# Optimization experiments

Hardware: AMD Instinct MI355X
Metric: run time of the kernel (lower is better)

## Reference

```python
import jax, jax.numpy as jnp
import numpy as np

B, N, H, R = 128, 512, 256, 3
VIRTUAL_DECAY = 0.7


def _build_tree():
    # Deterministic random recursive tree: parent[i] ~ U[0, i)
    rng = np.random.default_rng(0)
    parent = np.zeros(N, np.int64)
    for i in range(1, N):
        parent[i] = rng.integers(0, i)
    depth = np.zeros(N, np.int64)
    for i in range(1, N):
        depth[i] = depth[parent[i]] + 1
    rel_edge = rng.integers(0, R, N)          # relation type of edge (parent -> i)
    virtual = rng.random(N) < 0.1
    children = [[] for _ in range(N)]
    for i in range(1, N):
        children[parent[i]].append(i)
    # Group internal nodes by depth (deepest first == valid post-order batching),
    # pad ragged child lists per level.
    levels = []
    for d in range(int(depth.max()), -1, -1):
        nodes = [n for n in range(N) if depth[n] == d and len(children[n]) > 0]
        if not nodes:
            continue
        cmax = max(len(children[n]) for n in nodes)
        M = len(nodes)
        cidx = np.zeros((M, cmax), np.int64)
        cmask = np.zeros((M, cmax), np.float32)
        crel = np.zeros((M, cmax), np.int64)
        cvirt = np.zeros((M, cmax), bool)
        for m, n in enumerate(nodes):
            ch = children[n]
            k = len(ch)
            cidx[m, :k] = ch
            cmask[m, :k] = 1.0
            crel[m, :k] = rel_edge[ch]
            cvirt[m, :k] = virtual[ch]
        levels.append((jnp.array(nodes), jnp.array(cidx), jnp.array(cmask),
                       jnp.array(crel), jnp.array(cvirt)))
    return levels

LEVELS = _build_tree()


def _forward(node_features, W_enc, b_enc, rel_emb, W_i, b_i, W_o, b_o, W_u, b_u,
             W_f, b_f, w_attn, b_attn):
    h = node_features @ W_enc + b_enc            # (B, N, H) node_encoder
    c = jnp.zeros_like(h)
    for node_ids, cidx, cmask, crel, cvirt in LEVELS:
        x = h[:, node_ids]                       # (B, M, H) input_vec (== encoded feats)
        ch_h = h[:, cidx]                        # (B, M, C, H)
        ch_c = c[:, cidx]
        # virtual-node decay + padding mask
        decay = jnp.where(cvirt, VIRTUAL_DECAY, 1.0).astype(h.dtype) * cmask  # (M, C)
        ch_h = ch_h * decay[None, :, :, None]
        ch_c = ch_c * decay[None, :, :, None]
        # relation-aware attention over children
        re = rel_emb[crel]                       # (M, C, H)
        scores = jnp.einsum('bmch,h->bmc', re[None] + ch_h, w_attn) + b_attn[0]
        scores = jnp.where(cmask[None] > 0, scores, -1e9)
        attw = jax.nn.softmax(scores, axis=-1)   # (B, M, C)
        h_sum = jnp.einsum('bmc,bmch->bmh', attw, ch_h)
        # per-relation forget transform (note: original applies NO sigmoid here)
        f = jnp.zeros_like(ch_h)
        for r in range(R):
            fr = jnp.einsum('bmch,hk->bmck', ch_h, W_f[r]) + b_f[r]
            f = f + fr * (crel == r).astype(h.dtype)[None, :, :, None]
        c_sum = jnp.sum(f * ch_c, axis=2)        # (B, M, H); padded ch_c is 0
        comb = jnp.concatenate([x, h_sum], axis=-1)  # (B, M, 2H)
        i_g = jax.nn.sigmoid(comb @ W_i + b_i)
        o_g = jax.nn.sigmoid(comb @ W_o + b_o)
        u_g = jnp.tanh(comb @ W_u + b_u)
        c_new = i_g * u_g + c_sum
        h_new = o_g * jnp.tanh(c_new)
        h = h.at[:, node_ids].set(h_new)
        c = c.at[:, node_ids].set(c_new)
    return h[:, 0]                               # pooling == 'root' (root = 0)


def setup_inputs() -> dict:
    key = jax.random.key(0)
    ks = jax.random.split(key, 8)
    s = 0.05
    f32 = jnp.float32
    return {
        'node_features': jax.random.normal(ks[0], (B, N, H), f32),
        'W_enc': jax.random.normal(ks[1], (H, H), f32) * s,
        'b_enc': jnp.full((H,), 0.1, f32),
        'rel_emb': jax.random.normal(ks[2], (R, H), f32) * s,
        'W_i': jax.random.normal(ks[3], (2 * H, H), f32) * s,
        'b_i': jnp.full((H,), 0.1, f32),
        'W_o': jax.random.normal(ks[4], (2 * H, H), f32) * s,
        'b_o': jnp.full((H,), 0.1, f32),
        'W_u': jax.random.normal(ks[5], (2 * H, H), f32) * s,
        'b_u': jnp.full((H,), 0.1, f32),
        'W_f': jax.random.normal(ks[6], (R, H, H), f32) * s,
        'b_f': jnp.full((R, H), 0.1, f32),
        'w_attn': jax.random.normal(ks[7], (H,), f32) * s,
        'b_attn': jnp.full((1,), 0.1, f32),
    }


def reference(node_features, W_enc, b_enc, rel_emb, W_i, b_i, W_o, b_o, W_u, b_u,
              W_f, b_f, w_attn, b_attn):
    return _forward(node_features, W_enc, b_enc, rel_emb, W_i, b_i, W_o, b_o,
                    W_u, b_u, W_f, b_f, w_attn, b_attn)
```

## Files before the change

kernel.cpp:

```cpp
#include <hip/hip_runtime.h>
#include <stdint.h>
#include <string.h>
#include <math.h>

#define NB 128
#define NN 512
#define NH 256
#define NR 3

typedef __attribute__((ext_vector_type(8))) short bh8;
typedef __attribute__((ext_vector_type(4))) float f32x4;

struct Pcg {
  __uint128_t state, inc;
  bool has32; uint32_t buf32;
};

static const __uint128_t PCG_MULT =
    (((__uint128_t)2549297995355413924ULL) << 64) | 4865540595714422341ULL;

static inline uint64_t pcg_next64(Pcg& s) {
  s.state = s.state * PCG_MULT + s.inc;
  uint64_t hi = (uint64_t)(s.state >> 64), lo = (uint64_t)s.state;
  uint64_t x = hi ^ lo;
  unsigned rot = (unsigned)(s.state >> 122) & 63u;
  return (x >> rot) | (x << ((64u - rot) & 63u));
}
static inline uint32_t pcg_next32(Pcg& s) {
  if (s.has32) { s.has32 = false; return s.buf32; }
  uint64_t n = pcg_next64(s);
  s.has32 = true; s.buf32 = (uint32_t)(n >> 32);
  return (uint32_t)n;
}
static inline uint64_t pcg_bounded(Pcg& s, uint64_t high) {
  uint64_t rng = high - 1;
  if (rng == 0) return 0;
  uint32_t rng_excl = (uint32_t)rng + 1u;
  uint64_t m = (uint64_t)pcg_next32(s) * (uint64_t)rng_excl;
  uint32_t leftover = (uint32_t)m;
  if (leftover < rng_excl) {
    uint32_t threshold = (uint32_t)((0xFFFFFFFFu - (uint32_t)rng) % rng_excl);
    while (leftover < threshold) {
      m = (uint64_t)pcg_next32(s) * (uint64_t)rng_excl;
      leftover = (uint32_t)m;
    }
  }
  return m >> 32;
}
static inline double pcg_double(Pcg& s) {
  return (double)(pcg_next64(s) >> 11) * (1.0 / 9007199254740992.0);
}

static void pcg_seed0(Pcg& s) {
  uint32_t pool[4];
  uint32_t hc = 0x43b0d7e5u;
  auto hashmix = [&hc](uint32_t v) -> uint32_t {
    v ^= hc; hc *= 0x931e8875u; v *= hc; v ^= v >> 16; return v;
  };
  auto mix = [](uint32_t x, uint32_t y) -> uint32_t {
    uint32_t r = 0xca01f9ddu * x - 0x4973f715u * y; r ^= r >> 16; return r;
  };
  for (int i = 0; i < 4; i++) pool[i] = hashmix(0u);
  for (int src = 0; src < 4; src++)
    for (int dst = 0; dst < 4; dst++)
      if (src != dst) pool[dst] = mix(pool[dst], hashmix(pool[src]));
  uint32_t gs[8]; uint32_t hb = 0x8b51f9ddu;
  for (int i = 0; i < 8; i++) {
    uint32_t dv = pool[i & 3];
    dv ^= hb; hb *= 0x58f38dedu; dv *= hb; dv ^= dv >> 16;
    gs[i] = dv;
  }
  uint64_t w0 = (uint64_t)gs[0] | ((uint64_t)gs[1] << 32);
  uint64_t w1 = (uint64_t)gs[2] | ((uint64_t)gs[3] << 32);
  uint64_t w2 = (uint64_t)gs[4] | ((uint64_t)gs[5] << 32);
  uint64_t w3 = (uint64_t)gs[6] | ((uint64_t)gs[7] << 32);
  __uint128_t initstate = (((__uint128_t)w0) << 64) | w1;
  __uint128_t initseq   = (((__uint128_t)w2) << 64) | w3;
  s.state = 0;
  s.inc = (initseq << 1) | 1;
  s.state = s.state * PCG_MULT + s.inc;
  s.state += initstate;
  s.state = s.state * PCG_MULT + s.inc;
  s.has32 = false; s.buf32 = 0;
}

struct TreeMeta {
  int nodes[512];
  int cstart[512];
  int ccount[512];
  int echild[512];
  int erel[512];
  float edecay[512];
  int cechild[512];
  int cerel[512];
  float cedec[512];
  int cens[513];
};
struct HostTree {
  TreeMeta meta;
  int n_levels;
  int level_off[520];
  int level_M[520];
};

static void build_tree_host(HostTree& T) {
  Pcg st; pcg_seed0(st);
  int parent[NN], depth[NN], rel[NN];
  unsigned char virt[NN];
  parent[0] = 0; depth[0] = 0;
  for (int i = 1; i < NN; i++) parent[i] = (int)pcg_bounded(st, (uint64_t)i);
  for (int i = 1; i < NN; i++) depth[i] = depth[parent[i]] + 1;
  for (int i = 0; i < NN; i++) rel[i] = (int)pcg_bounded(st, (uint64_t)NR);
  for (int i = 0; i < NN; i++) virt[i] = (pcg_double(st) < 0.1) ? 1 : 0;

  int childcnt[NN]; memset(childcnt, 0, sizeof(childcnt));
  for (int i = 1; i < NN; i++) childcnt[parent[i]]++;
  int maxd = 0;
  for (int i = 0; i < NN; i++) if (depth[i] > maxd) maxd = depth[i];

  int ni = 0, ne = 0, nec = 0;
  T.n_levels = 0;
  for (int d = maxd; d >= 0; d--) {
    int mstart = ni;
    for (int n = 0; n < NN; n++) {
      if (depth[n] == d && childcnt[n] > 0) {
        T.meta.nodes[ni] = n;
        T.meta.cstart[ni] = ne;
        T.meta.ccount[ni] = childcnt[n];
        T.meta.cens[ni] = nec;
        for (int i2 = 1; i2 < NN; i2++) {
          if (parent[i2] == n) {
            T.meta.echild[ne] = i2;
            T.meta.erel[ne] = rel[i2];
            T.meta.edecay[ne] = virt[i2] ? 0.7f : 1.0f;
            ne++;
            if (childcnt[i2] > 0) {
              T.meta.cechild[nec] = i2;
              T.meta.cerel[nec] = rel[i2];
              T.meta.cedec[nec] = virt[i2] ? 0.7f : 1.0f;
              nec++;
            }
          }
        }
        ni++;
      }
    }
    if (ni > mstart) {
      T.level_off[T.n_levels] = mstart;
      T.level_M[T.n_levels] = ni - mstart;
      T.n_levels++;
    }
  }
  T.meta.cens[ni] = nec;
}

__device__ __forceinline__ uint16_t f2bf(float f) {
  uint32_t u = __float_as_uint(f);
  return (uint16_t)((u + 0x7fffu + ((u >> 16) & 1u)) >> 16);
}
__device__ __forceinline__ float bf2f(uint16_t b) {
  return __uint_as_float(((uint32_t)b) << 16);
}
__device__ __forceinline__ float sigm(float x) {
  return 1.f / (1.f + expf(-x));
}

__device__ __forceinline__ void stage_bf16(uint16_t* __restrict__ sm,
    const uint16_t* __restrict__ src, int stride, int rows) {
  const int chunks = rows << 3;
  for (int cch = threadIdx.x; cch < chunks; cch += 256) {
    const int row = cch >> 3, k = (cch & 7) << 3;
    uint4 v = *(const uint4*)(src + (size_t)row * stride + k);
    *(uint4*)(sm + (((row << 6) + k) ^ ((row & 7) << 3))) = v;
  }
}
__device__ __forceinline__ void stage_f32(uint16_t* __restrict__ sm,
    const float* __restrict__ src, int stride, int rows) {
  const int chunks = rows << 3;
  for (int cch = threadIdx.x; cch < chunks; cch += 256) {
    const int row = cch >> 3, k = (cch & 7) << 3;
    const float* p = src + (size_t)row * stride + k;
    float4 a = *(const float4*)p, b = *(const float4*)(p + 4);
    uint4 w;
    w.x = (uint32_t)f2bf(a.x) | ((uint32_t)f2bf(a.y) << 16);
    w.y = (uint32_t)f2bf(a.z) | ((uint32_t)f2bf(a.w) << 16);
    w.z = (uint32_t)f2bf(b.x) | ((uint32_t)f2bf(b.y) << 16);
    w.w = (uint32_t)f2bf(b.z) | ((uint32_t)f2bf(b.w) << 16);
    *(uint4*)(sm + (((row << 6) + k) ^ ((row & 7) << 3))) = w;
  }
}
__device__ __forceinline__ bh8 fld(const uint16_t* __restrict__ sm, int row, int k) {
  return *(const bh8*)(sm + (((row << 6) + k) ^ ((row & 7) << 3)));
}

__global__ __launch_bounds__(256) void k_prep(const float* __restrict__ We,
    const float* __restrict__ Wf, const float* __restrict__ Wi,
    const float* __restrict__ Wo, const float* __restrict__ Wu,
    uint16_t* __restrict__ WeT, uint16_t* __restrict__ WfT,
    uint16_t* __restrict__ WgT) {
  const int i = blockIdx.x * 256 + threadIdx.x;
  if (i < 65536) {
    const int n = i >> 8, k = i & 255;
    WeT[i] = f2bf(We[k * 256 + n]);
  }
  const int i2 = i - 65536;
  if (i2 >= 0 && i2 < 196608) {
    const int r = i2 >> 16, rem = i2 & 65535, n = rem >> 8, k = rem & 255;
    WfT[i2] = f2bf(Wf[r * 65536 + k * 256 + n]);
  }
  const int i3 = i - 262144;
  if (i3 >= 0 && i3 < 393216) {
    const int g = i3 >> 17, rem = i3 & 131071, n = rem >> 9, k = rem & 511;
    const float* S = (g == 0) ? Wi : (g == 1) ? Wo : Wu;
    WgT[i3] = f2bf(S[k * 256 + n]);
  }
}

__global__ __launch_bounds__(256) void k_enc(const float* __restrict__ nf,
    const uint16_t* __restrict__ WeT, const float* __restrict__ b_enc,
    uint16_t* __restrict__ h_bf) {
  __shared__ __align__(16) uint16_t smA[128 * 64];
  __shared__ __align__(16) uint16_t smB[128 * 64];
  const int bm = blockIdx.x * 128, bn = blockIdx.y * 128;
  const int tid = threadIdx.x, wid = tid >> 6, lane = tid & 63;
  const int wr = wid >> 1, wc2 = wid & 1, lr = lane & 15, lk = (lane >> 4) << 3;
  f32x4 acc[4][4] = {};
  for (int k0 = 0; k0 < 256; k0 += 64) {
    __syncthreads();
    stage_f32(smA, nf + (size_t)bm * NH + k0, NH, 128);
    stage_bf16(smB, WeT + (size_t)bn * 256 + k0, 256, 128);
    __syncthreads();
#pragma unroll
    for (int ks = 0; ks < 2; ks++) {
      bh8 af[4], bfr[4];
#pragma unroll
      for (int i = 0; i < 4; i++) af[i] = fld(smA, wr * 64 + i * 16 + lr, ks * 32 + lk);
#pragma unroll
      for (int j = 0; j < 4; j++) bfr[j] = fld(smB, wc2 * 64 + j * 16 + lr, ks * 32 + lk);
#pragma unroll
      for (int i = 0; i < 4; i++)
#pragma unroll
        for (int j = 0; j < 4; j++)
          acc[i][j] = __builtin_amdgcn_mfma_f32_16x16x32_bf16(af[i], bfr[j], acc[i][j], 0, 0, 0);
    }
  }
#pragma unroll
  for (int i = 0; i < 4; i++) {
#pragma unroll
    for (int j = 0; j < 4; j++) {
      const int col = bn + wc2 * 64 + j * 16 + (lane & 15);
      const float be = b_enc[col];
#pragma unroll
      for (int r = 0; r < 4; r++) {
        const int row = bm + wr * 64 + i * 16 + (lane >> 4) * 4 + r;
        h_bf[(size_t)row * NH + col] = f2bf(acc[i][j][r] + be);
      }
    }
  }
}

__global__ __launch_bounds__(256) void k_lvl(
    uint16_t* h_bf, float* c,
    const uint16_t* __restrict__ WfT, const uint16_t* __restrict__ WgT,
    const float* __restrict__ b_f, const float* __restrict__ b_i,
    const float* __restrict__ b_o, const float* __restrict__ b_u,
    const float* __restrict__ rel_emb, const float* __restrict__ w_attn,
    const float* __restrict__ b_attn, float* __restrict__ out,
    const TreeMeta* __restrict__ tm, int nb) {
  __shared__ float sc[64 * 65];
  __shared__ float swa[256];
  __shared__ float sRE[3];
  __shared__ int chl[64]; __shared__ int rll[64]; __shared__ float dcl[64];
  __shared__ __align__(16) uint16_t hsum[4 * 4096];

  const int bx = blockIdx.x, mloc = bx >> 1, b0 = (bx & 1) * 64;
  const int cslice = blockIdx.y * 64;
  const int gi = nb + mloc;
  const int nd = tm->nodes[gi], cs = tm->cstart[gi], cc = tm->ccount[gi];
  const int ce0 = tm->cens[gi], nic = tm->cens[gi + 1] - ce0;
  const int tid = threadIdx.x, wid = tid >> 6, lane = tid & 63;
  const int lr2 = lane & 15, hi4 = (lane >> 4), lk = hi4 << 3;
  const int colw = cslice + wid * 16 + lr2;

  if (tid < cc) {
    chl[tid] = tm->echild[cs + tid];
    rll[tid] = tm->erel[cs + tid];
    dcl[tid] = tm->edecay[cs + tid];
  }
  swa[tid] = w_attn[tid];
  if (wid < 3) {
    float p = 0.f;
#pragma unroll
    for (int i = 0; i < 4; i++) p += rel_emb[wid * NH + lane + 64 * i] * w_attn[lane + 64 * i];
#pragma unroll
    for (int off = 32; off; off >>= 1) p += __shfl_down(p, off);
    if (lane == 0) sRE[wid] = p;
  }
  __syncthreads();

  const int sb = tid >> 2, sq = tid & 3;
  const float ba = b_attn[0];
  for (int e = 0; e < cc; e++) {
    const uint16_t* hp = h_bf + ((size_t)(b0 + sb) * NN + chl[e]) * NH + sq * 64;
    float s = 0.f;
#pragma unroll
    for (int v = 0; v < 8; v++) {
      uint4 pk = *(const uint4*)(hp + v * 8);
      const uint16_t* pe = (const uint16_t*)&pk;
#pragma unroll
      for (int q = 0; q < 8; q++) s = fmaf(bf2f(pe[q]), swa[sq * 64 + v * 8 + q], s);
    }
    s += __shfl_xor(s, 1); s += __shfl_xor(s, 2);
    if (sq == 0) sc[sb * 65 + e] = sRE[rll[e]] + dcl[e] * s + ba;
  }
  __syncthreads();
  if (tid < 64) {
    float mx = -1e30f;
    for (int e = 0; e < cc; e++) mx = fmaxf(mx, sc[tid * 65 + e]);
    float ss = 0.f;
    for (int e = 0; e < cc; e++) ss += expf(sc[tid * 65 + e] - mx);
    const float inv = 1.0f / ss;
    for (int e = 0; e < cc; e++) sc[tid * 65 + e] = expf(sc[tid * 65 + e] - mx) * inv * dcl[e];
  }
  __syncthreads();

  {
    float hs[64];
#pragma unroll
    for (int v = 0; v < 64; v++) hs[v] = 0.f;
    for (int e = 0; e < cc; e++) {
      const float w = sc[sb * 65 + e];
      const uint16_t* hp = h_bf + ((size_t)(b0 + sb) * NN + chl[e]) * NH + sq * 64;
#pragma unroll
      for (int v = 0; v < 8; v++) {
        uint4 pk = *(const uint4*)(hp + v * 8);
        const uint16_t* pe = (const uint16_t*)&pk;
#pragma unroll
        for (int q = 0; q < 8; q++) hs[v * 8 + q] = fmaf(bf2f(pe[q]), w, hs[v * 8 + q]);
      }
    }
    uint16_t* sub = hsum + sq * 4096;
#pragma unroll
    for (int v = 0; v < 32; v++) {
      uint32_t pk = (uint32_t)f2bf(hs[2 * v]) | ((uint32_t)f2bf(hs[2 * v + 1]) << 16);
      const int elem = ((sb << 6) + 2 * v) ^ ((sb & 7) << 3);
      *(uint32_t*)(sub + elem) = pk;
    }
  }

  f32x4 csum[4] = {};
  for (int e = 0; e < nic; e++) {
    const int ch = tm->cechild[ce0 + e];
    const int rel = tm->cerel[ce0 + e];
    const float dec = tm->cedec[ce0 + e];
    const uint16_t* Wr = WfT + (size_t)rel * 65536 + (size_t)colw * 256;
    f32x4 facc[4] = {};
#pragma unroll
    for (int k0 = 0; k0 < 8; k0++) {
      const int kk = k0 * 32 + lk;
      bh8 af[4];
#pragma unroll
      for (int i = 0; i < 4; i++)
        af[i] = *(const bh8*)(h_bf + ((size_t)(b0 + i * 16 + lr2) * NN + ch) * NH + kk);
      const bh8 bq = *(const bh8*)(Wr + kk);
#pragma unroll
      for (int i = 0; i < 4; i++)
        facc[i] = __builtin_amdgcn_mfma_f32_16x16x32_bf16(af[i], bq, facc[i], 0, 0, 0);
    }
    const float bfv = b_f[rel * NH + colw];
#pragma unroll
    for (int i = 0; i < 4; i++) {
#pragma unroll
      for (int r = 0; r < 4; r++) {
        const int brow = b0 + i * 16 + hi4 * 4 + r;
        const float cch = c[((size_t)brow * NN + ch) * NH + colw];
        csum[i][r] += (dec * facc[i][r] + bfv) * (dec * cch);
      }
    }
  }
  __syncthreads();

  f32x4 ga[3][4] = {};
#pragma unroll
  for (int k32 = 0; k32 < 16; k32++) {
    const int kk = k32 * 32 + lk;
    bh8 af[4], bq[3];
    if (k32 < 8) {
#pragma unroll
      for (int i = 0; i < 4; i++)
        af[i] = *(const bh8*)(h_bf + ((size_t)(b0 + i * 16 + lr2) * NN + nd) * NH + kk);
    } else {
      const int kx = k32 - 8;
#pragma unroll
      for (int i = 0; i < 4; i++)
        af[i] = fld(hsum + (kx >> 1) * 4096, i * 16 + lr2, (kx & 1) * 32 + lk);
    }
#pragma unroll
    for (int g = 0; g < 3; g++)
      bq[g] = *(const bh8*)(WgT + ((size_t)g << 17) + (size_t)colw * 512 + kk);
#pragma unroll
    for (int g = 0; g < 3; g++)
#pragma unroll
      for (int i = 0; i < 4; i++)
        ga[g][i] = __builtin_amdgcn_mfma_f32_16x16x32_bf16(af[i], bq[g], ga[g][i], 0, 0, 0);
  }

  const float bi_ = b_i[colw], bo_ = b_o[colw], bu_ = b_u[colw];
#pragma unroll
  for (int i = 0; i < 4; i++) {
#pragma unroll
    for (int r = 0; r < 4; r++) {
      const int brow = b0 + i * 16 + hi4 * 4 + r;
      const size_t idx = ((size_t)brow * NN + nd) * NH + colw;
      const float ig = sigm(ga[0][i][r] + bi_);
      const float og = sigm(ga[1][i][r] + bo_);
      const float ug = tanhf(ga[2][i][r] + bu_);
      const float cn = fmaf(ig, ug, csum[i][r]);
      c[idx] = cn;
      const float hn = og * tanhf(cn);
      h_bf[idx] = f2bf(hn);
      if (nd == 0) out[(size_t)brow * NH + colw] = hn;
    }
  }
}

extern "C" void kernel_launch(void* const* d_in, const int* in_sizes, int n_in,
                              void* d_out, int out_size, void* d_ws, size_t ws_size,
                              hipStream_t stream) {
  (void)in_sizes; (void)n_in; (void)out_size; (void)ws_size;
  const float* nf      = (const float*)d_in[0];
  const float* W_enc   = (const float*)d_in[1];
  const float* b_enc   = (const float*)d_in[2];
  const float* rel_emb = (const float*)d_in[3];
  const float* W_i     = (const float*)d_in[4];
  const float* b_i     = (const float*)d_in[5];
  const float* W_o     = (const float*)d_in[6];
  const float* b_o     = (const float*)d_in[7];
  const float* W_u     = (const float*)d_in[8];
  const float* b_u     = (const float*)d_in[9];
  const float* W_f     = (const float*)d_in[10];
  const float* b_f     = (const float*)d_in[11];
  const float* w_attn  = (const float*)d_in[12];
  const float* b_attn  = (const float*)d_in[13];
  float* out = (float*)d_out;

  static HostTree T;
  build_tree_host(T);

  char* ws = (char*)d_ws;
  const size_t OFF_HBF = 32768;
  const size_t SZ_HBF  = (size_t)NB * NN * NH * 2;
  const size_t OFF_WET = OFF_HBF + SZ_HBF;
  const size_t OFF_WFT = OFF_WET + 131072;
  const size_t OFF_WGT = OFF_WFT + 393216;
  const size_t OFF_C   = OFF_WGT + 786432;

  TreeMeta* dm = (TreeMeta*)ws;
  uint16_t* h_bf = (uint16_t*)(ws + OFF_HBF);
  uint16_t* WeT = (uint16_t*)(ws + OFF_WET);
  uint16_t* WfT = (uint16_t*)(ws + OFF_WFT);
  uint16_t* WgT = (uint16_t*)(ws + OFF_WGT);
  float* c = (float*)(ws + OFF_C);

  hipMemcpyAsync(dm, &T.meta, sizeof(TreeMeta), hipMemcpyHostToDevice, stream);

  k_prep<<<2560, 256, 0, stream>>>(W_enc, W_f, W_i, W_o, W_u, WeT, WfT, WgT);
  k_enc<<<dim3((NB * NN) / 128, 2), 256, 0, stream>>>(nf, WeT, b_enc, h_bf);

  for (int l = 0; l < T.n_levels; l++) {
    const int Mfull = T.level_M[l];
    for (int c0 = 0; c0 < Mfull; c0 += 128) {
      const int Mc = (Mfull - c0) < 128 ? (Mfull - c0) : 128;
      k_lvl<<<dim3(2 * Mc, 4), 256, 0, stream>>>(h_bf, c, WfT, WgT,
          b_f, b_i, b_o, b_u, rel_emb, w_attn, b_attn, out, dm,
          T.level_off[l] + c0);
    }
  }
}
```

Before: 735.5 us.

## Fuse small tree levels into one persistent tail kernel processing nodes sequentially

Consecutive levels with fewer than TH_TAIL internal nodes are handled by a new k_tail kernel, launched with 8 blocks of 16 batch rows each. Each block loops over those nodes in dependency order, computing the attention scores, the softmax-weighted child sum, the forget-gate cell sum and the gate GEMMs inside one launch. The aim is to remove the per-level launch overhead and the underutilised tiny grids of the top levels of the tree. In exchange, the tail runs on only 8 workgroups and processes its nodes serially, with repeated weight reads from global memory.

```diff
diff --git a/kernel.cpp b/kernel.cpp
--- a/kernel.cpp
+++ b/kernel.cpp
@@ -7,6 +7,7 @@
 #define NN 512
 #define NH 256
 #define NR 3
+#define TH_TAIL 10
 
 typedef __attribute__((ext_vector_type(8))) short bh8;
 typedef __attribute__((ext_vector_type(4))) float f32x4;
@@ -424,6 +425,182 @@
   }
 }
 
+__global__ __launch_bounds__(256) void k_tail(
+    uint16_t* h_bf, float* c,
+    const uint16_t* __restrict__ WfT, const uint16_t* __restrict__ WgT,
+    const float* __restrict__ b_f, const float* __restrict__ b_i,
+    const float* __restrict__ b_o, const float* __restrict__ b_u,
+    const float* __restrict__ rel_emb, const float* __restrict__ w_attn,
+    const float* __restrict__ b_attn, float* __restrict__ out,
+    const TreeMeta* __restrict__ tm, int start, int count) {
+  __shared__ float sc[16 * 68];
+  __shared__ float swaf[256];
+  __shared__ float sRE[3];
+  __shared__ int chl[64]; __shared__ int rll[64]; __shared__ float dcl[64];
+  __shared__ __align__(16) uint16_t hsum[16 * 256];
+
+  const int tid = threadIdx.x, wid = tid >> 6, lane = tid & 63;
+  const int b0 = blockIdx.x * 16;
+  const int lb = lane & 15, lq = lane >> 4;
+
+  swaf[tid] = w_attn[tid];
+  if (wid < 3) {
+    float p = 0.f;
+#pragma unroll
+    for (int i = 0; i < 4; i++) p += rel_emb[wid * NH + lane + 64 * i] * w_attn[lane + 64 * i];
+#pragma unroll
+    for (int off = 32; off; off >>= 1) p += __shfl_down(p, off);
+    if (lane == 0) sRE[wid] = p;
+  }
+  const float ba = b_attn[0];
+
+  for (int n = 0; n < count; n++) {
+    const int gi = start + n;
+    const int nd = tm->nodes[gi], cs = tm->cstart[gi], cc = tm->ccount[gi];
+    const int ce0 = tm->cens[gi], nic = tm->cens[gi + 1] - ce0;
+    if (tid < cc) {
+      chl[tid] = tm->echild[cs + tid];
+      rll[tid] = tm->erel[cs + tid];
+      dcl[tid] = tm->edecay[cs + tid];
+    }
+    __syncthreads();
+
+    for (int e = wid; e < cc; e += 4) {
+      const uint16_t* hp = h_bf + ((size_t)(b0 + lb) * NN + chl[e]) * NH + lq * 64;
+      float s = 0.f;
+#pragma unroll
+      for (int v = 0; v < 8; v++) {
+        bh8 hv = *(const bh8*)(hp + v * 8);
+        const float4 w0 = *(const float4*)(swaf + lq * 64 + v * 8);
+        const float4 w1 = *(const float4*)(swaf + lq * 64 + v * 8 + 4);
+        s = fmaf(bf2f((uint16_t)hv[0]), w0.x, s);
+        s = fmaf(bf2f((uint16_t)hv[1]), w0.y, s);
+        s = fmaf(bf2f((uint16_t)hv[2]), w0.z, s);
+        s = fmaf(bf2f((uint16_t)hv[3]), w0.w, s);
+        s = fmaf(bf2f((uint16_t)hv[4]), w1.x, s);
+        s = fmaf(bf2f((uint16_t)hv[5]), w1.y, s);
+        s = fmaf(bf2f((uint16_t)hv[6]), w1.z, s);
+        s = fmaf(bf2f((uint16_t)hv[7]), w1.w, s);
+      }
+      s += __shfl_xor(s, 16); s += __shfl_xor(s, 32);
+      if (lq == 0) sc[lb * 68 + e] = sRE[rll[e]] + dcl[e] * s + ba;
+    }
+    __syncthreads();
+    if (tid < 16) {
+      float mx = -1e30f;
+      for (int e = 0; e < cc; e++) mx = fmaxf(mx, sc[tid * 68 + e]);
+      float ss = 0.f;
+      for (int e = 0; e < cc; e++) ss += expf(sc[tid * 68 + e] - mx);
+      const float inv = 1.0f / ss;
+      for (int e = 0; e < cc; e++) sc[tid * 68 + e] = expf(sc[tid * 68 + e] - mx) * inv * dcl[e];
+    }
+    __syncthreads();
+
+    {
+      const int b = tid & 15, q = tid >> 4;
+      float hs[16];
+#pragma unroll
+      for (int u = 0; u < 16; u++) hs[u] = 0.f;
+      for (int e = 0; e < cc; e++) {
+        const float w = sc[b * 68 + e];
+        const uint16_t* hp = h_bf + ((size_t)(b0 + b) * NN + chl[e]) * NH + q * 16;
+        uint4 p0 = *(const uint4*)(hp);
+        uint4 p1 = *(const uint4*)(hp + 8);
+        const uint16_t* e0 = (const uint16_t*)&p0;
+        const uint16_t* e1 = (const uint16_t*)&p1;
+#pragma unroll
+        for (int u = 0; u < 8; u++) hs[u] = fmaf(bf2f(e0[u]), w, hs[u]);
+#pragma unroll
+        for (int u = 0; u < 8; u++) hs[8 + u] = fmaf(bf2f(e1[u]), w, hs[8 + u]);
+      }
+      uint16_t* sub = hsum + (q >> 2) * 1024;
+#pragma unroll
+      for (int v = 0; v < 8; v++) {
+        uint32_t pk = (uint32_t)f2bf(hs[2 * v]) | ((uint32_t)f2bf(hs[2 * v + 1]) << 16);
+        const int elem = ((b << 6) + (q & 3) * 16 + 2 * v) ^ ((b & 7) << 3);
+        *(uint32_t*)(sub + elem) = pk;
+      }
+    }
+
+    f32x4 csum[4] = {};
+    for (int e = 0; e < nic; e++) {
+      const int ch = tm->cechild[ce0 + e];
+      const int rel = tm->cerel[ce0 + e];
+      const float dec = tm->cedec[ce0 + e];
+      const uint16_t* hrow = h_bf + ((size_t)(b0 + lb) * NN + ch) * NH;
+      const uint16_t* Wr = WfT + (size_t)rel * 65536;
+      f32x4 facc[4] = {};
+#pragma unroll
+      for (int k0 = 0; k0 < 8; k0++) {
+        const int kk = k0 * 32 + lq * 8;
+        const bh8 af = *(const bh8*)(hrow + kk);
+        bh8 bq[4];
+#pragma unroll
+        for (int j = 0; j < 4; j++)
+          bq[j] = *(const bh8*)(Wr + (size_t)(wid * 64 + j * 16 + lb) * 256 + kk);
+#pragma unroll
+        for (int j = 0; j < 4; j++)
+          facc[j] = __builtin_amdgcn_mfma_f32_16x16x32_bf16(af, bq[j], facc[j], 0, 0, 0);
+      }
+#pragma unroll
+      for (int j = 0; j < 4; j++) {
+        const int col = wid * 64 + j * 16 + lb;
+        const float bfv = b_f[rel * NH + col];
+#pragma unroll
+        for (int r = 0; r < 4; r++) {
+          const int brow = b0 + lq * 4 + r;
+          const float cch = c[((size_t)brow * NN + ch) * NH + col];
+          csum[j][r] += (dec * facc[j][r] + bfv) * (dec * cch);
+        }
+      }
+    }
+    __syncthreads();
+
+    f32x4 ga[3][4] = {};
+    const uint16_t* xrow = h_bf + ((size_t)(b0 + lb) * NN + nd) * NH;
+#pragma unroll
+    for (int k32 = 0; k32 < 16; k32++) {
+      const int kk = k32 * 32 + lq * 8;
+      bh8 af;
+      if (k32 < 8) {
+        af = *(const bh8*)(xrow + kk);
+      } else {
+        const int kx = k32 - 8;
+        const int elem = ((lb << 6) + (kx & 1) * 32 + lq * 8) ^ ((lb & 7) << 3);
+        af = *(const bh8*)(hsum + (kx >> 1) * 1024 + elem);
+      }
+#pragma unroll
+      for (int g = 0; g < 3; g++) {
+#pragma unroll
+        for (int j = 0; j < 4; j++) {
+          const bh8 bq = *(const bh8*)(WgT + ((size_t)g << 17) +
+                                       (size_t)(wid * 64 + j * 16 + lb) * 512 + k32 * 32 + lq * 8);
+          ga[g][j] = __builtin_amdgcn_mfma_f32_16x16x32_bf16(af, bq, ga[g][j], 0, 0, 0);
+        }
+      }
+    }
+#pragma unroll
+    for (int j = 0; j < 4; j++) {
+      const int col = wid * 64 + j * 16 + lb;
+      const float bi_ = b_i[col], bo_ = b_o[col], bu_ = b_u[col];
+#pragma unroll
+      for (int r = 0; r < 4; r++) {
+        const int brow = b0 + lq * 4 + r;
+        const size_t idx = ((size_t)brow * NN + nd) * NH + col;
+        const float ig = sigm(ga[0][j][r] + bi_);
+        const float og = sigm(ga[1][j][r] + bo_);
+        const float ug = tanhf(ga[2][j][r] + bu_);
+        const float cn = fmaf(ig, ug, csum[j][r]);
+        c[idx] = cn;
+        const float hn = og * tanhf(cn);
+        h_bf[idx] = f2bf(hn);
+        if (nd == 0) out[(size_t)brow * NH + col] = hn;
+      }
+    }
+    __syncthreads();
+  }
+}
+
 extern "C" void kernel_launch(void* const* d_in, const int* in_sizes, int n_in,
                               void* d_out, int out_size, void* d_ws, size_t ws_size,
                               hipStream_t stream) {
@@ -467,13 +644,24 @@
   k_prep<<<2560, 256, 0, stream>>>(W_enc, W_f, W_i, W_o, W_u, WeT, WfT, WgT);
   k_enc<<<dim3((NB * NN) / 128, 2), 256, 0, stream>>>(nf, WeT, b_enc, h_bf);
 
-  for (int l = 0; l < T.n_levels; l++) {
-    const int Mfull = T.level_M[l];
-    for (int c0 = 0; c0 < Mfull; c0 += 128) {
-      const int Mc = (Mfull - c0) < 128 ? (Mfull - c0) : 128;
-      k_lvl<<<dim3(2 * Mc, 4), 256, 0, stream>>>(h_bf, c, WfT, WgT,
+  int l = 0;
+  while (l < T.n_levels) {
+    if (T.level_M[l] >= TH_TAIL) {
+      const int Mfull = T.level_M[l];
+      for (int c0 = 0; c0 < Mfull; c0 += 128) {
+        const int Mc = (Mfull - c0) < 128 ? (Mfull - c0) : 128;
+        k_lvl<<<dim3(2 * Mc, 4), 256, 0, stream>>>(h_bf, c, WfT, WgT,
+            b_f, b_i, b_o, b_u, rel_emb, w_attn, b_attn, out, dm,
+            T.level_off[l] + c0);
+      }
+      l++;
+    } else {
+      int j = l, cnt = 0;
+      while (j < T.n_levels && T.level_M[j] < TH_TAIL) { cnt += T.level_M[j]; j++; }
+      k_tail<<<dim3(8), 256, 0, stream>>>(h_bf, c, WfT, WgT,
           b_f, b_i, b_o, b_u, rel_emb, w_attn, b_attn, out, dm,
-          T.level_off[l] + c0);
-    }
-  }
-}
+          T.level_off[l], cnt);
+      l = j;
+    }
+  }
+}
```

Result: slower. 1.558 ms (+111.9%).

## Add narrow-column kernel for tree levels with few nodes

Applied to the files above, without the earlier changes.

Adds a k_tiny kernel for levels with fewer than eight nodes. It splits the hidden dimension into sixteen 16-column blocks per node and 64-row batch halves, so a small level launches more workgroups. Each block recomputes the attention scores and weighted child sum for its batch rows, then does the forget-gate and gate GEMMs only for its 16 columns. This trades redundant attention and child-sum work for better GPU occupancy on the many sequential, nearly serial top levels of the tree.

```diff
diff --git a/kernel.cpp b/kernel.cpp
--- a/kernel.cpp
+++ b/kernel.cpp
@@ -7,6 +7,7 @@
 #define NN 512
 #define NH 256
 #define NR 3
+#define TH_TINY 8
 
 typedef __attribute__((ext_vector_type(8))) short bh8;
 typedef __attribute__((ext_vector_type(4))) float f32x4;
@@ -424,6 +425,154 @@
   }
 }
 
+__global__ __launch_bounds__(256) void k_tiny(
+    uint16_t* h_bf, float* c,
+    const uint16_t* __restrict__ WfT, const uint16_t* __restrict__ WgT,
+    const float* __restrict__ b_f, const float* __restrict__ b_i,
+    const float* __restrict__ b_o, const float* __restrict__ b_u,
+    const float* __restrict__ rel_emb, const float* __restrict__ w_attn,
+    const float* __restrict__ b_attn, float* __restrict__ out,
+    const TreeMeta* __restrict__ tm, int nb) {
+  __shared__ float sc[64 * 65];
+  __shared__ float swa[256];
+  __shared__ float sRE[3];
+  __shared__ int chl[64]; __shared__ int rll[64]; __shared__ float dcl[64];
+  __shared__ __align__(16) uint16_t hsum[4 * 4096];
+
+  const int c0 = blockIdx.x * 16;
+  const int mloc = blockIdx.y >> 1, b0 = (blockIdx.y & 1) * 64;
+  const int gi = nb + mloc;
+  const int nd = tm->nodes[gi], cs = tm->cstart[gi], cc = tm->ccount[gi];
+  const int ce0 = tm->cens[gi], nic = tm->cens[gi + 1] - ce0;
+  const int tid = threadIdx.x, wid = tid >> 6, lane = tid & 63;
+  const int lb = lane & 15, lq = lane >> 4;
+  const int colw = c0 + lb;
+  const int wrow = b0 + wid * 16;
+
+  if (tid < cc) {
+    chl[tid] = tm->echild[cs + tid];
+    rll[tid] = tm->erel[cs + tid];
+    dcl[tid] = tm->edecay[cs + tid];
+  }
+  swa[tid] = w_attn[tid];
+  if (wid < 3) {
+    float p = 0.f;
+#pragma unroll
+    for (int i = 0; i < 4; i++) p += rel_emb[wid * NH + lane + 64 * i] * w_attn[lane + 64 * i];
+#pragma unroll
+    for (int off = 32; off; off >>= 1) p += __shfl_down(p, off);
+    if (lane == 0) sRE[wid] = p;
+  }
+  __syncthreads();
+
+  const int sb = tid >> 2, sq = tid & 3;
+  const float ba = b_attn[0];
+  for (int e = 0; e < cc; e++) {
+    const uint16_t* hp = h_bf + ((size_t)(b0 + sb) * NN + chl[e]) * NH + sq * 64;
+    float s = 0.f;
+#pragma unroll
+    for (int v = 0; v < 8; v++) {
+      uint4 pk = *(const uint4*)(hp + v * 8);
+      const uint16_t* pe = (const uint16_t*)&pk;
+#pragma unroll
+      for (int q = 0; q < 8; q++) s = fmaf(bf2f(pe[q]), swa[sq * 64 + v * 8 + q], s);
+    }
+    s += __shfl_xor(s, 1); s += __shfl_xor(s, 2);
+    if (sq == 0) sc[sb * 65 + e] = sRE[rll[e]] + dcl[e] * s + ba;
+  }
+  __syncthreads();
+  if (tid < 64) {
+    float mx = -1e30f;
+    for (int e = 0; e < cc; e++) mx = fmaxf(mx, sc[tid * 65 + e]);
+    float ss = 0.f;
+    for (int e = 0; e < cc; e++) ss += expf(sc[tid * 65 + e] - mx);
+    const float inv = 1.0f / ss;
+    for (int e = 0; e < cc; e++) sc[tid * 65 + e] = expf(sc[tid * 65 + e] - mx) * inv * dcl[e];
+  }
+  __syncthreads();
+
+  {
+    float hs[64];
+#pragma unroll
+    for (int v = 0; v < 64; v++) hs[v] = 0.f;
+    for (int e = 0; e < cc; e++) {
+      const float w = sc[sb * 65 + e];
+      const uint16_t* hp = h_bf + ((size_t)(b0 + sb) * NN + chl[e]) * NH + sq * 64;
+#pragma unroll
+      for (int v = 0; v < 8; v++) {
+        uint4 pk = *(const uint4*)(hp + v * 8);
+        const uint16_t* pe = (const uint16_t*)&pk;
+#pragma unroll
+        for (int q = 0; q < 8; q++) hs[v * 8 + q] = fmaf(bf2f(pe[q]), w, hs[v * 8 + q]);
+      }
+    }
+    uint16_t* sub = hsum + sq * 4096;
+#pragma unroll
+    for (int v = 0; v < 32; v++) {
+      uint32_t pk = (uint32_t)f2bf(hs[2 * v]) | ((uint32_t)f2bf(hs[2 * v + 1]) << 16);
+      const int elem = ((sb << 6) + 2 * v) ^ ((sb & 7) << 3);
+      *(uint32_t*)(sub + elem) = pk;
+    }
+  }
+
+  f32x4 csum = {};
+  for (int e = 0; e < nic; e++) {
+    const int ch = tm->cechild[ce0 + e];
+    const int rel = tm->cerel[ce0 + e];
+    const float dec = tm->cedec[ce0 + e];
+    const uint16_t* Wr = WfT + (size_t)rel * 65536 + (size_t)colw * 256;
+    f32x4 facc = {};
+#pragma unroll
+    for (int k0 = 0; k0 < 8; k0++) {
+      const int kk = k0 * 32 + lq * 8;
+      const bh8 af = *(const bh8*)(h_bf + ((size_t)(wrow + lb) * NN + ch) * NH + kk);
+      const bh8 bq = *(const bh8*)(Wr + kk);
+      facc = __builtin_amdgcn_mfma_f32_16x16x32_bf16(af, bq, facc, 0, 0, 0);
+    }
+    const float bfv = b_f[rel * NH + colw];
+#pragma unroll
+    for (int r = 0; r < 4; r++) {
+      const int brow = wrow + lq * 4 + r;
+      const float cch = c[((size_t)brow * NN + ch) * NH + colw];
+      csum[r] += (dec * facc[r] + bfv) * (dec * cch);
+    }
+  }
+  __syncthreads();
+
+  f32x4 ga[3] = {};
+#pragma unroll
+  for (int k32 = 0; k32 < 16; k32++) {
+    const int kk = k32 * 32 + lq * 8;
+    bh8 af;
+    if (k32 < 8) {
+      af = *(const bh8*)(h_bf + ((size_t)(wrow + lb) * NN + nd) * NH + kk);
+    } else {
+      const int kx = k32 - 8;
+      af = fld(hsum + (kx >> 1) * 4096, wid * 16 + lb, (kx & 1) * 32 + lq * 8);
+    }
+#pragma unroll
+    for (int g = 0; g < 3; g++) {
+      const bh8 bq = *(const bh8*)(WgT + ((size_t)g << 17) + (size_t)colw * 512 + kk);
+      ga[g] = __builtin_amdgcn_mfma_f32_16x16x32_bf16(af, bq, ga[g], 0, 0, 0);
+    }
+  }
+
+  const float bi_ = b_i[colw], bo_ = b_o[colw], bu_ = b_u[colw];
+#pragma unroll
+  for (int r = 0; r < 4; r++) {
+    const int brow = wrow + lq * 4 + r;
+    const size_t idx = ((size_t)brow * NN + nd) * NH + colw;
+    const float ig = sigm(ga[0][r] + bi_);
+    const float og = sigm(ga[1][r] + bo_);
+    const float ug = tanhf(ga[2][r] + bu_);
+    const float cn = fmaf(ig, ug, csum[r]);
+    c[idx] = cn;
+    const float hn = og * tanhf(cn);
+    h_bf[idx] = f2bf(hn);
+    if (nd == 0) out[(size_t)brow * NH + colw] = hn;
+  }
+}
+
 extern "C" void kernel_launch(void* const* d_in, const int* in_sizes, int n_in,
                               void* d_out, int out_size, void* d_ws, size_t ws_size,
                               hipStream_t stream) {
@@ -469,11 +618,17 @@
 
   for (int l = 0; l < T.n_levels; l++) {
     const int Mfull = T.level_M[l];
-    for (int c0 = 0; c0 < Mfull; c0 += 128) {
-      const int Mc = (Mfull - c0) < 128 ? (Mfull - c0) : 128;
-      k_lvl<<<dim3(2 * Mc, 4), 256, 0, stream>>>(h_bf, c, WfT, WgT,
+    if (Mfull >= TH_TINY) {
+      for (int c0 = 0; c0 < Mfull; c0 += 128) {
+        const int Mc = (Mfull - c0) < 128 ? (Mfull - c0) : 128;
+        k_lvl<<<dim3(2 * Mc, 4), 256, 0, stream>>>(h_bf, c, WfT, WgT,
+            b_f, b_i, b_o, b_u, rel_emb, w_attn, b_attn, out, dm,
+            T.level_off[l] + c0);
+      }
+    } else {
+      k_tiny<<<dim3(16, 2 * Mfull), 256, 0, stream>>>(h_bf, c, WfT, WgT,
           b_f, b_i, b_o, b_u, rel_emb, w_attn, b_attn, out, dm,
-          T.level_off[l] + c0);
-    }
-  }
-}
+          T.level_off[l]);
+    }
+  }
+}
```

New measurement: 682.0 us. 1.08x faster.

## Retile level kernel into 16-column slices, precompute attention partials, double-buffer child loads

Applied to the files above, without the earlier changes.

The per-level kernel is split into 16 column slices of 16 columns each instead of 4 slices of 64. That gives many more blocks per level, and each wave now issues a single MFMA row tile. Attention scores are no longer recomputed from full child h vectors: k_sv0 precomputes per-16-column partial dot products, and the epilogue of each level updates them for the new node. A separate x_enc copy of the encoded features is read for the gate inputs, which avoids reading h entries that other column blocks are overwriting. The weighted child-sum loop double-buffers its row loads. In exchange it adds a workspace buffer, an extra pre-pass and more redundant weight reads across blocks.

```diff
diff --git a/kernel.cpp b/kernel.cpp
--- a/kernel.cpp
+++ b/kernel.cpp
@@ -193,6 +193,16 @@
   return *(const bh8*)(sm + (((row << 6) + k) ^ ((row & 7) << 3)));
 }
 
+#define LDROW(BUF, CH) do { \
+    const uint4* p_ = (const uint4*)(hbase + (size_t)(CH) * NH); \
+    BUF[0]=p_[0]; BUF[1]=p_[1]; BUF[2]=p_[2]; BUF[3]=p_[3]; \
+    BUF[4]=p_[4]; BUF[5]=p_[5]; BUF[6]=p_[6]; BUF[7]=p_[7]; } while (0)
+#define ACCROW(BUF, W) do { const float w_ = (W); \
+    _Pragma("unroll") for (int v_ = 0; v_ < 8; v_++) { \
+      const uint16_t* pe_ = (const uint16_t*)&BUF[v_]; \
+      _Pragma("unroll") for (int q_ = 0; q_ < 8; q_++) \
+        hs[v_*8+q_] = fmaf(bf2f(pe_[q_]), w_, hs[v_*8+q_]); } } while (0)
+
 __global__ __launch_bounds__(256) void k_prep(const float* __restrict__ We,
     const float* __restrict__ Wf, const float* __restrict__ Wi,
     const float* __restrict__ Wo, const float* __restrict__ Wu,
@@ -218,7 +228,7 @@
 
 __global__ __launch_bounds__(256) void k_enc(const float* __restrict__ nf,
     const uint16_t* __restrict__ WeT, const float* __restrict__ b_enc,
-    uint16_t* __restrict__ h_bf) {
+    uint16_t* __restrict__ h_bf, uint16_t* __restrict__ x_enc) {
   __shared__ __align__(16) uint16_t smA[128 * 64];
   __shared__ __align__(16) uint16_t smB[128 * 64];
   const int bm = blockIdx.x * 128, bn = blockIdx.y * 128;
@@ -253,14 +263,34 @@
 #pragma unroll
       for (int r = 0; r < 4; r++) {
         const int row = bm + wr * 64 + i * 16 + (lane >> 4) * 4 + r;
-        h_bf[(size_t)row * NH + col] = f2bf(acc[i][j][r] + be);
+        const uint16_t hv = f2bf(acc[i][j][r] + be);
+        h_bf[(size_t)row * NH + col] = hv;
+        x_enc[(size_t)row * NH + col] = hv;
       }
     }
   }
 }
 
-__global__ __launch_bounds__(256) void k_lvl(
-    uint16_t* h_bf, float* c,
+__global__ __launch_bounds__(256) void k_sv0(const uint16_t* __restrict__ h_bf,
+    const float* __restrict__ w_attn, float* __restrict__ svp) {
+  const int idx = blockIdx.x * 256 + threadIdx.x;
+  const int g = idx & 15;
+  const size_t row = (size_t)(idx >> 4);
+  const uint16_t* hp = h_bf + row * NH + g * 16;
+  uint4 p0 = *(const uint4*)hp, p1 = *(const uint4*)(hp + 8);
+  const uint16_t* e0 = (const uint16_t*)&p0;
+  const uint16_t* e1 = (const uint16_t*)&p1;
+  float s = 0.f;
+#pragma unroll
+  for (int u = 0; u < 8; u++) s = fmaf(bf2f(e0[u]), w_attn[g * 16 + u], s);
+#pragma unroll
+  for (int u = 0; u < 8; u++) s = fmaf(bf2f(e1[u]), w_attn[g * 16 + 8 + u], s);
+  svp[idx] = s;
+}
+
+__global__ __launch_bounds__(256) void k_tiny(
+    uint16_t* h_bf, float* c, float* __restrict__ svp,
+    const uint16_t* __restrict__ x_enc,
     const uint16_t* __restrict__ WfT, const uint16_t* __restrict__ WgT,
     const float* __restrict__ b_f, const float* __restrict__ b_i,
     const float* __restrict__ b_o, const float* __restrict__ b_u,
@@ -273,14 +303,15 @@
   __shared__ int chl[64]; __shared__ int rll[64]; __shared__ float dcl[64];
   __shared__ __align__(16) uint16_t hsum[4 * 4096];
 
-  const int bx = blockIdx.x, mloc = bx >> 1, b0 = (bx & 1) * 64;
-  const int cslice = blockIdx.y * 64;
+  const int c0 = blockIdx.x * 16;
+  const int mloc = blockIdx.y >> 1, b0 = (blockIdx.y & 1) * 64;
   const int gi = nb + mloc;
   const int nd = tm->nodes[gi], cs = tm->cstart[gi], cc = tm->ccount[gi];
   const int ce0 = tm->cens[gi], nic = tm->cens[gi + 1] - ce0;
   const int tid = threadIdx.x, wid = tid >> 6, lane = tid & 63;
-  const int lr2 = lane & 15, hi4 = (lane >> 4), lk = hi4 << 3;
-  const int colw = cslice + wid * 16 + lr2;
+  const int lb = lane & 15, lq = lane >> 4;
+  const int colw = c0 + lb;
+  const int wrow = b0 + wid * 16;
 
   if (tid < cc) {
     chl[tid] = tm->echild[cs + tid];
@@ -298,23 +329,16 @@
   }
   __syncthreads();
 
-  const int sb = tid >> 2, sq = tid & 3;
   const float ba = b_attn[0];
-  for (int e = 0; e < cc; e++) {
-    const uint16_t* hp = h_bf + ((size_t)(b0 + sb) * NN + chl[e]) * NH + sq * 64;
-    float s = 0.f;
-#pragma unroll
-    for (int v = 0; v < 8; v++) {
-      uint4 pk = *(const uint4*)(hp + v * 8);
-      const uint16_t* pe = (const uint16_t*)&pk;
-#pragma unroll
-      for (int q = 0; q < 8; q++) s = fmaf(bf2f(pe[q]), swa[sq * 64 + v * 8 + q], s);
-    }
-    s += __shfl_xor(s, 1); s += __shfl_xor(s, 2);
-    if (sq == 0) sc[sb * 65 + e] = sRE[rll[e]] + dcl[e] * s + ba;
-  }
-  __syncthreads();
   if (tid < 64) {
+    const float* svpb = svp + (size_t)(b0 + tid) * NN * 16;
+    for (int e = 0; e < cc; e++) {
+      const float4* p = (const float4*)(svpb + chl[e] * 16);
+      float4 a = p[0], b2 = p[1], c2 = p[2], d2 = p[3];
+      float s = ((a.x + a.y) + (a.z + a.w)) + ((b2.x + b2.y) + (b2.z + b2.w)) +
+                ((c2.x + c2.y) + (c2.z + c2.w)) + ((d2.x + d2.y) + (d2.z + d2.w));
+      sc[tid * 65 + e] = sRE[rll[e]] + dcl[e] * s + ba;
+    }
     float mx = -1e30f;
     for (int e = 0; e < cc; e++) mx = fmaxf(mx, sc[tid * 65 + e]);
     float ss = 0.f;
@@ -324,21 +348,22 @@
   }
   __syncthreads();
 
+  const int sb = tid >> 2, sq = tid & 3;
   {
     float hs[64];
 #pragma unroll
     for (int v = 0; v < 64; v++) hs[v] = 0.f;
-    for (int e = 0; e < cc; e++) {
-      const float w = sc[sb * 65 + e];
-      const uint16_t* hp = h_bf + ((size_t)(b0 + sb) * NN + chl[e]) * NH + sq * 64;
-#pragma unroll
-      for (int v = 0; v < 8; v++) {
-        uint4 pk = *(const uint4*)(hp + v * 8);
-        const uint16_t* pe = (const uint16_t*)&pk;
-#pragma unroll
-        for (int q = 0; q < 8; q++) hs[v * 8 + q] = fmaf(bf2f(pe[q]), w, hs[v * 8 + q]);
-      }
-    }
+    const uint16_t* hbase = h_bf + (size_t)(b0 + sb) * NN * NH + sq * 64;
+    uint4 bufA[8], bufB[8];
+    LDROW(bufA, chl[0]);
+    int e = 0;
+    for (; e + 2 <= cc; e += 2) {
+      LDROW(bufB, chl[e + 1]);
+      ACCROW(bufA, sc[sb * 65 + e]);
+      if (e + 2 < cc) LDROW(bufA, chl[e + 2]);
+      ACCROW(bufB, sc[sb * 65 + e + 1]);
+    }
+    if (e < cc) ACCROW(bufA, sc[sb * 65 + e]);
     uint16_t* sub = hsum + sq * 4096;
 #pragma unroll
     for (int v = 0; v < 32; v++) {
@@ -348,79 +373,67 @@
     }
   }
 
-  f32x4 csum[4] = {};
+  f32x4 csum = {};
+#pragma unroll 2
   for (int e = 0; e < nic; e++) {
     const int ch = tm->cechild[ce0 + e];
     const int rel = tm->cerel[ce0 + e];
     const float dec = tm->cedec[ce0 + e];
     const uint16_t* Wr = WfT + (size_t)rel * 65536 + (size_t)colw * 256;
-    f32x4 facc[4] = {};
+    f32x4 facc = {};
 #pragma unroll
     for (int k0 = 0; k0 < 8; k0++) {
-      const int kk = k0 * 32 + lk;
-      bh8 af[4];
-#pragma unroll
-      for (int i = 0; i < 4; i++)
-        af[i] = *(const bh8*)(h_bf + ((size_t)(b0 + i * 16 + lr2) * NN + ch) * NH + kk);
+      const int kk = k0 * 32 + lq * 8;
+      const bh8 af = *(const bh8*)(h_bf + ((size_t)(wrow + lb) * NN + ch) * NH + kk);
       const bh8 bq = *(const bh8*)(Wr + kk);
-#pragma unroll
-      for (int i = 0; i < 4; i++)
-        facc[i] = __builtin_amdgcn_mfma_f32_16x16x32_bf16(af[i], bq, facc[i], 0, 0, 0);
+      facc = __builtin_amdgcn_mfma_f32_16x16x32_bf16(af, bq, facc, 0, 0, 0);
     }
     const float bfv = b_f[rel * NH + colw];
 #pragma unroll
-    for (int i = 0; i < 4; i++) {
-#pragma unroll
-      for (int r = 0; r < 4; r++) {
-        const int brow = b0 + i * 16 + hi4 * 4 + r;
-        const float cch = c[((size_t)brow * NN + ch) * NH + colw];
-        csum[i][r] += (dec * facc[i][r] + bfv) * (dec * cch);
-      }
+    for (int r = 0; r < 4; r++) {
+      const int brow = wrow + lq * 4 + r;
+      const float cch = c[((size_t)brow * NN + ch) * NH + colw];
+      csum[r] += (dec * facc[r] + bfv) * (dec * cch);
     }
   }
   __syncthreads();
 
-  f32x4 ga[3][4] = {};
+  f32x4 ga[3] = {};
 #pragma unroll
   for (int k32 = 0; k32 < 16; k32++) {
-    const int kk = k32 * 32 + lk;
-    bh8 af[4], bq[3];
+    const int kk = k32 * 32 + lq * 8;
+    bh8 af;
     if (k32 < 8) {
-#pragma unroll
-      for (int i = 0; i < 4; i++)
-        af[i] = *(const bh8*)(h_bf + ((size_t)(b0 + i * 16 + lr2) * NN + nd) * NH + kk);
+      af = *(const bh8*)(x_enc + ((size_t)(wrow + lb) * NN + nd) * NH + kk);
     } else {
       const int kx = k32 - 8;
-#pragma unroll
-      for (int i = 0; i < 4; i++)
-        af[i] = fld(hsum + (kx >> 1) * 4096, i * 16 + lr2, (kx & 1) * 32 + lk);
-    }
-#pragma unroll
-    for (int g = 0; g < 3; g++)
-      bq[g] = *(const bh8*)(WgT + ((size_t)g << 17) + (size_t)colw * 512 + kk);
-#pragma unroll
-    for (int g = 0; g < 3; g++)
-#pragma unroll
-      for (int i = 0; i < 4; i++)
-        ga[g][i] = __builtin_amdgcn_mfma_f32_16x16x32_bf16(af[i], bq[g], ga[g][i], 0, 0, 0);
+      af = fld(hsum + (kx >> 1) * 4096, wid * 16 + lb, (kx & 1) * 32 + lq * 8);
+    }
+#pragma unroll
+    for (int g = 0; g < 3; g++) {
+      const bh8 bq = *(const bh8*)(WgT + ((size_t)g << 17) + (size_t)colw * 512 + kk);
+      ga[g] = __builtin_amdgcn_mfma_f32_16x16x32_bf16(af, bq, ga[g], 0, 0, 0);
+    }
   }
 
   const float bi_ = b_i[colw], bo_ = b_o[colw], bu_ = b_u[colw];
-#pragma unroll
-  for (int i = 0; i < 4; i++) {
-#pragma unroll
-    for (int r = 0; r < 4; r++) {
-      const int brow = b0 + i * 16 + hi4 * 4 + r;
-      const size_t idx = ((size_t)brow * NN + nd) * NH + colw;
-      const float ig = sigm(ga[0][i][r] + bi_);
-      const float og = sigm(ga[1][i][r] + bo_);
-      const float ug = tanhf(ga[2][i][r] + bu_);
-      const float cn = fmaf(ig, ug, csum[i][r]);
-      c[idx] = cn;
-      const float hn = og * tanhf(cn);
-      h_bf[idx] = f2bf(hn);
-      if (nd == 0) out[(size_t)brow * NH + colw] = hn;
-    }
+  const float wac = swa[colw];
+#pragma unroll
+  for (int r = 0; r < 4; r++) {
+    const int brow = wrow + lq * 4 + r;
+    const size_t idx = ((size_t)brow * NN + nd) * NH + colw;
+    const float ig = sigm(ga[0][r] + bi_);
+    const float og = sigm(ga[1][r] + bo_);
+    const float ug = tanhf(ga[2][r] + bu_);
+    const float cn = fmaf(ig, ug, csum[r]);
+    c[idx] = cn;
+    const float hn = og * tanhf(cn);
+    h_bf[idx] = f2bf(hn);
+    if (nd == 0) out[(size_t)brow * NH + colw] = hn;
+    float pv = hn * wac;
+    pv += __shfl_xor(pv, 1); pv += __shfl_xor(pv, 2);
+    pv += __shfl_xor(pv, 4); pv += __shfl_xor(pv, 8);
+    if (lb == 0) svp[((size_t)brow * NN + nd) * 16 + (c0 >> 4)] = pv;
   }
 }
 
@@ -450,30 +463,32 @@
   char* ws = (char*)d_ws;
   const size_t OFF_HBF = 32768;
   const size_t SZ_HBF  = (size_t)NB * NN * NH * 2;
-  const size_t OFF_WET = OFF_HBF + SZ_HBF;
+  const size_t OFF_XE  = OFF_HBF + SZ_HBF;
+  const size_t OFF_WET = OFF_XE + SZ_HBF;
   const size_t OFF_WFT = OFF_WET + 131072;
   const size_t OFF_WGT = OFF_WFT + 393216;
   const size_t OFF_C   = OFF_WGT + 786432;
+  const size_t SZ_C    = (size_t)NB * NN * NH * 4;
+  const size_t OFF_SVP = OFF_C + SZ_C;
 
   TreeMeta* dm = (TreeMeta*)ws;
   uint16_t* h_bf = (uint16_t*)(ws + OFF_HBF);
+  uint16_t* x_enc = (uint16_t*)(ws + OFF_XE);
   uint16_t* WeT = (uint16_t*)(ws + OFF_WET);
   uint16_t* WfT = (uint16_t*)(ws + OFF_WFT);
   uint16_t* WgT = (uint16_t*)(ws + OFF_WGT);
   float* c = (float*)(ws + OFF_C);
+  float* svp = (float*)(ws + OFF_SVP);
 
   hipMemcpyAsync(dm, &T.meta, sizeof(TreeMeta), hipMemcpyHostToDevice, stream);
 
   k_prep<<<2560, 256, 0, stream>>>(W_enc, W_f, W_i, W_o, W_u, WeT, WfT, WgT);
-  k_enc<<<dim3((NB * NN) / 128, 2), 256, 0, stream>>>(nf, WeT, b_enc, h_bf);
+  k_enc<<<dim3((NB * NN) / 128, 2), 256, 0, stream>>>(nf, WeT, b_enc, h_bf, x_enc);
+  k_sv0<<<dim3((NB * NN * 16) / 256), 256, 0, stream>>>(h_bf, w_attn, svp);
 
   for (int l = 0; l < T.n_levels; l++) {
-    const int Mfull = T.level_M[l];
-    for (int c0 = 0; c0 < Mfull; c0 += 128) {
-      const int Mc = (Mfull - c0) < 128 ? (Mfull - c0) : 128;
-      k_lvl<<<dim3(2 * Mc, 4), 256, 0, stream>>>(h_bf, c, WfT, WgT,
-          b_f, b_i, b_o, b_u, rel_emb, w_attn, b_attn, out, dm,
-          T.level_off[l] + c0);
-    }
-  }
-}
+    k_tiny<<<dim3(16, 2 * T.level_M[l]), 256, 0, stream>>>(h_bf, c, svp, x_enc,
+        WfT, WgT, b_f, b_i, b_o, b_u, rel_emb, w_attn, b_attn, out, dm,
+        T.level_off[l]);
+  }
+}
```

New measurement: 653.6 us. 1.13x faster.
